# Kernel tuning notes

Measured on AMD Instinct MI355X. Metric: run time of the kernel, lower is better.

## Reference

```python
import jax, jax.numpy as jnp
import numpy as np

B = 262144
C = 128
NUM_CLASSES = 128   # fill_max for y
PAD = 2048
EPS = 1e-8
REJECT_THRESHOLD = 1


def setup_inputs() -> dict:
    key = jax.random.key(0)
    kx, ky = jax.random.split(key)
    x = jax.random.normal(kx, (B, C), dtype=jnp.float32)
    y = jax.random.randint(ky, (B,), 0, NUM_CLASSES)
    return {"x": x, "y": y}


def _decorrelate_loss(x, y):
    Bn, Cn = x.shape
    # per-class counts / sums (segment reduce replaces the python loop + boolean mask)
    counts = jax.ops.segment_sum(jnp.ones((Bn,), x.dtype), y, num_segments=NUM_CLASSES)  # [K]
    counts_i = counts.astype(jnp.int32)
    sums = jax.ops.segment_sum(x, y, num_segments=NUM_CLASSES)                            # [K, C]
    mean = sums / jnp.maximum(counts, 1.0)[:, None]
    centered = x - mean[y]                                                                # [B, C]
    # unbiased variance per class (torch .var default), guarded for count<=1
    var = jax.ops.segment_sum(centered * centered, y, num_segments=NUM_CLASSES) \
        / jnp.maximum(counts - 1.0, 1.0)[:, None]                                         # [K, C]
    xn = centered / jnp.sqrt(EPS + var)[y]                                                # [B, C]
    # sort rows by class so each class occupies a contiguous block, then slice fixed-size
    order = jnp.argsort(y)
    xs = jnp.concatenate([xn[order], jnp.zeros((PAD, Cn), x.dtype)], axis=0)              # [B+PAD, C]
    cum = jnp.cumsum(counts_i)
    starts = jnp.concatenate([jnp.zeros((1,), jnp.int32), cum[:-1]])                      # exclusive cumsum
    gathered = jax.vmap(lambda s: jax.lax.dynamic_slice(xs, (s, 0), (PAD, Cn)))(starts)   # [K, PAD, C]
    row_valid = (jnp.arange(PAD)[None, :] < counts_i[:, None]).astype(x.dtype)            # [K, PAD]
    g = gathered * row_valid[:, :, None]
    # per-class correlation matrices, all at once
    corr = jnp.einsum('kpc,kpd->kcd', g, g)                                               # [K, C, C]
    sq_sum = jnp.sum(corr * corr, axis=(1, 2))                                            # [K]
    diag_sq = jnp.sum(jnp.einsum('kcc->kc', corr) ** 2, axis=1)                           # [K]
    off_mean = (sq_sum - diag_sq) / (Cn * (Cn - 1))                                       # off_diagonal(.)^2 mean
    valid = counts_i > REJECT_THRESHOLD
    loss = jnp.sum(jnp.where(valid, off_mean, 0.0))
    n_count = jnp.sum(jnp.where(valid, counts, 0.0))
    return jnp.where(n_count > 0, loss / n_count, 0.0)


def reference(x, y):
    return _decorrelate_loss(x, y)
```

## Files before the change

### kernel.cpp

```cpp
#include <hip/hip_runtime.h>

#define B_ROWS   262144
#define C_DIM    128
#define K_CLS    128
#define PAD_R    2048
#define PAD2     4096
#define EPS_F    1e-8f
#define CHUNK    1024
#define G_CHUNKS 256

typedef float f32x4  __attribute__((ext_vector_type(4)));
typedef short bf16x8 __attribute__((ext_vector_type(8)));

__device__ __forceinline__ unsigned f2bf(float f) {
  unsigned u = __float_as_uint(f);
  return (u + 0x7fffu + ((u >> 16) & 1u)) >> 16;
}
__device__ __forceinline__ unsigned packbf(float a, float b) {
  return f2bf(a) | (f2bf(b) << 16);
}
__device__ __forceinline__ int swzkey(int c) { return (c ^ (c >> 2)) & 7; }

__global__ __launch_bounds__(256) void hist_kernel(const int* __restrict__ y,
                                                   int* __restrict__ hist) {
  __shared__ int h[K_CLS];
  int g = blockIdx.x, tid = threadIdx.x;
  if (tid < K_CLS) h[tid] = 0;
  __syncthreads();
  for (int j = tid; j < CHUNK; j += 256) atomicAdd(&h[y[g * CHUNK + j]], 1);
  __syncthreads();
  if (tid < K_CLS) hist[g * K_CLS + tid] = h[tid];
}

__global__ __launch_bounds__(256) void scan_kernel(int* __restrict__ hist,
                                                   int* __restrict__ counts) {
  __shared__ int s[G_CHUNKS];
  int k = blockIdx.x, g = threadIdx.x;
  int v = hist[g * K_CLS + k];
  s[g] = v;
  __syncthreads();
  for (int off = 1; off < G_CHUNKS; off <<= 1) {
    int t = (g >= off) ? s[g - off] : 0;
    __syncthreads();
    s[g] += t;
    __syncthreads();
  }
  hist[g * K_CLS + k] = s[g] - v;
  if (g == G_CHUNKS - 1) counts[k] = s[g];
}

__global__ __launch_bounds__(256) void rank_kernel(const int* __restrict__ y,
                                                   const int* __restrict__ hist,
                                                   int* __restrict__ ord) {
  __shared__ unsigned short cnt_sub[16][K_CLS];
  __shared__ int offs[K_CLS];
  const int g = blockIdx.x, tid = threadIdx.x;
  const int lane = tid & 63, w = tid >> 6;
  if (tid < K_CLS) offs[tid] = hist[g * K_CLS + tid];
  {
    unsigned int* cz = (unsigned int*)cnt_sub;
    for (int i = tid; i < 16 * K_CLS / 2; i += 256) cz[i] = 0;
  }
  __syncthreads();

  int yv[4], rig[4];
  #pragma unroll
  for (int i = 0; i < 4; ++i) {
    const int s = w * 4 + i;
    const int yy = y[g * CHUNK + s * 64 + lane];
    unsigned long long m = ~0ULL;
    #pragma unroll
    for (int b = 0; b < 7; ++b) {
      unsigned long long bb = __ballot((yy >> b) & 1);
      m &= ((yy >> b) & 1) ? bb : ~bb;
    }
    const unsigned long long lt = (1ULL << lane) - 1ULL;
    rig[i] = (int)__popcll(m & lt);
    yv[i] = yy;
    const int leader = __ffsll((long long)m) - 1;
    if (lane == leader) cnt_sub[s][yy] = (unsigned short)__popcll(m);
  }
  __syncthreads();

  if (tid < K_CLS) {
    int run = 0;
    #pragma unroll
    for (int s = 0; s < 16; ++s) {
      int t = cnt_sub[s][tid];
      cnt_sub[s][tid] = (unsigned short)run;
      run += t;
    }
  }
  __syncthreads();

  #pragma unroll
  for (int i = 0; i < 4; ++i) {
    const int s = w * 4 + i;
    const int k = yv[i];
    const int R = offs[k] + (int)cnt_sub[s][k] + rig[i];
    if (R < PAD2) ord[k * PAD2 + R] = g * CHUNK + s * 64 + lane;
  }
}

__global__ __launch_bounds__(512, 1) void gemm_kernel(const float* __restrict__ x,
                                                      const int* __restrict__ ord,
                                                      const int* __restrict__ counts,
                                                      float* __restrict__ spart,
                                                      float* __restrict__ sums_part,
                                                      float* __restrict__ sqs_part,
                                                      float* __restrict__ ovfs_part) {
  __shared__ unsigned int lds[2 * C_DIM * 32];
  __shared__ int ord_l[PAD_R / 2];
  const int blk = blockIdx.x;
  const int k = blk >> 1, half = blk & 1;
  const int cnt_full = counts[k];
  const int T = cnt_full < PAD_R ? cnt_full : PAD_R;
  const int r_base = half * (PAD_R / 2);
  const int rend = (T < r_base + PAD_R / 2) ? T : (r_base + PAD_R / 2);
  const int nr = rend - r_base;
  const int nt = (nr > 0) ? ((nr + 63) >> 6) : 0;

  const int tid = threadIdx.x;
  const int lane = tid & 63;
  const int w = tid >> 6;
  const int wr = w >> 1, wc = w & 1;
  const int l5 = lane >> 5;
  const int lc = lane & 31;

  f32x4 acc[2][4];
  #pragma unroll
  for (int i = 0; i < 2; ++i)
    #pragma unroll
    for (int j = 0; j < 4; ++j) acc[i][j] = (f32x4){0.f, 0.f, 0.f, 0.f};
  float sum4[4] = {0.f, 0.f, 0.f, 0.f}, sq4[4] = {0.f, 0.f, 0.f, 0.f};

  const int* ordk = ord + k * PAD2;

  for (int i = tid; i < PAD_R / 2; i += 512) ord_l[i] = ordk[r_base + i];
  __syncthreads();

  auto load_tile = [&](int t, f32x4* vv) {
    const int rr = t * 64 + w * 8 + l5 * 4;
    const int4 idx = *(const int4*)(&ord_l[rr]);
    const int rg = r_base + rr;
    const size_t co = (size_t)(lc << 2);
    const f32x4 z = (f32x4){0.f, 0.f, 0.f, 0.f};
    vv[0] = (rg + 0 < rend) ? *(const f32x4*)(x + (size_t)idx.x * C_DIM + co) : z;
    vv[1] = (rg + 1 < rend) ? *(const f32x4*)(x + (size_t)idx.y * C_DIM + co) : z;
    vv[2] = (rg + 2 < rend) ? *(const f32x4*)(x + (size_t)idx.z * C_DIM + co) : z;
    vv[3] = (rg + 3 < rend) ? *(const f32x4*)(x + (size_t)idx.w * C_DIM + co) : z;
  };

  auto write_tile = [&](unsigned int* buf, const f32x4* vv) {
    #pragma unroll
    for (int j = 0; j < 4; ++j)
      #pragma unroll
      for (int e = 0; e < 4; ++e) { float t = vv[j][e]; sum4[e] += t; sq4[e] += t * t; }
    #pragma unroll
    for (int jp = 0; jp < 2; ++jp) {
      const int us = l5 * 2 + jp;
      #pragma unroll
      for (int e = 0; e < 4; ++e) {
        const int c = (lc << 2) + e;
        buf[c * 32 + (((w ^ swzkey(c)) << 2) | us)] =
            packbf(vv[jp * 2][e], vv[jp * 2 + 1][e]);
      }
    }
  };

  auto compute_tile = [&](const unsigned int* buf) {
    const int q2 = lane >> 4;
    const int fr = lane & 15;
    #pragma unroll
    for (int s = 0; s < 2; ++s) {
      const int g = s * 4 + q2;
      bf16x8 afr[2], bfr[4];
      #pragma unroll
      for (int mi = 0; mi < 2; ++mi) {
        const int c = wr * 32 + mi * 16 + fr;
        afr[mi] = *(const bf16x8*)(&buf[c * 32 + ((g ^ swzkey(c)) << 2)]);
      }
      #pragma unroll
      for (int ni = 0; ni < 4; ++ni) {
        const int d = wc * 64 + ni * 16 + fr;
        bfr[ni] = *(const bf16x8*)(&buf[d * 32 + ((g ^ swzkey(d)) << 2)]);
      }
      #pragma unroll
      for (int mi = 0; mi < 2; ++mi)
        #pragma unroll
        for (int ni = 0; ni < 4; ++ni)
          acc[mi][ni] = __builtin_amdgcn_mfma_f32_16x16x32_bf16(afr[mi], bfr[ni], acc[mi][ni], 0, 0, 0);
    }
  };

  f32x4 va[4], vb[4];
  if (nt > 0) { load_tile(0, va); write_tile(lds, va); }
  if (nt > 1) load_tile(1, va);
  __syncthreads();
  int cur = 0;
  for (int t = 0; t < nt; t += 2) {
    if (t + 1 < nt) write_tile(lds + (unsigned)(cur ^ 1) * (C_DIM * 32), va);
    if (t + 2 < nt) load_tile(t + 2, vb);
    compute_tile(lds + (unsigned)cur * (C_DIM * 32));
    __syncthreads();
    cur ^= 1;
    if (t + 1 >= nt) break;
    if (t + 2 < nt) write_tile(lds + (unsigned)(cur ^ 1) * (C_DIM * 32), vb);
    if (t + 3 < nt) load_tile(t + 3, va);
    compute_tile(lds + (unsigned)cur * (C_DIM * 32));
    __syncthreads();
    cur ^= 1;
  }

  float osum[4] = {0.f, 0.f, 0.f, 0.f}, osq[4] = {0.f, 0.f, 0.f, 0.f};
  const int colo = lc << 2;
  for (int r = PAD_R + half + ((tid >> 5) << 1); r < cnt_full; r += 32) {
    int row = ordk[r];
    f32x4 vv = *(const f32x4*)(x + (size_t)row * C_DIM + colo);
    #pragma unroll
    for (int e = 0; e < 4; ++e) { float t = vv[e]; osum[e] += t; osq[e] += t * t; }
  }

  __syncthreads();
  float* red = (float*)lds;
  if (tid < 3 * C_DIM) red[tid] = 0.f;
  __syncthreads();
  #pragma unroll
  for (int e = 0; e < 4; ++e) {
    atomicAdd(&red[colo + e], sum4[e]);
    atomicAdd(&red[C_DIM + colo + e], sq4[e] + osq[e]);
    atomicAdd(&red[2 * C_DIM + colo + e], osum[e]);
  }
  __syncthreads();
  if (tid < C_DIM) {
    sums_part[(half * K_CLS + k) * C_DIM + tid] = red[tid];
    sqs_part [(half * K_CLS + k) * C_DIM + tid] = red[C_DIM + tid];
    ovfs_part[(half * K_CLS + k) * C_DIM + tid] = red[2 * C_DIM + tid];
  }
  float* sp = spart + (size_t)(half * K_CLS + k) * (C_DIM * C_DIM);
  #pragma unroll
  for (int mi = 0; mi < 2; ++mi)
    #pragma unroll
    for (int ni = 0; ni < 4; ++ni)
      #pragma unroll
      for (int r = 0; r < 4; ++r) {
        int c = wr * 32 + mi * 16 + ((lane >> 4) << 2) + r;
        int d = wc * 64 + ni * 16 + (lane & 15);
        sp[c * C_DIM + d] = acc[mi][ni][r];
      }
}

__global__ __launch_bounds__(512) void finalize_kernel(const float* __restrict__ spart,
                                                       const float* __restrict__ sums_part,
                                                       const float* __restrict__ sqs_part,
                                                       const float* __restrict__ ovfs_part,
                                                       const int* __restrict__ counts,
                                                       float* __restrict__ numden) {
  __shared__ float m_l[C_DIM], is_l[C_DIM], st_l[C_DIM];
  __shared__ float wred[8];
  int k = blockIdx.x, tid = threadIdx.x;
  int count = counts[k];
  float Tf = (float)(count < PAD_R ? count : PAD_R);
  if (tid < C_DIM) {
    float s_tr = sums_part[k * C_DIM + tid] + sums_part[(K_CLS + k) * C_DIM + tid];
    float osum = ovfs_part[k * C_DIM + tid] + ovfs_part[(K_CLS + k) * C_DIM + tid];
    float fsum = s_tr + osum;
    float fsq  = sqs_part[k * C_DIM + tid] + sqs_part[(K_CLS + k) * C_DIM + tid];
    float cf = (float)count;
    float m = fsum / fmaxf(cf, 1.f);
    float var = (fsq - cf * m * m) / fmaxf(cf - 1.f, 1.f);
    m_l[tid] = m;
    is_l[tid] = rsqrtf(var + EPS_F);
    st_l[tid] = s_tr;
  }
  __syncthreads();
  const float* S0 = spart + (size_t)k * (C_DIM * C_DIM);
  const float* S1 = spart + (size_t)(K_CLS + k) * (C_DIM * C_DIM);
  float local = 0.f;
  for (int e4 = tid * 4; e4 < C_DIM * C_DIM; e4 += 512 * 4) {
    int c = e4 >> 7, d0 = e4 & 127;
    f32x4 s0 = *(const f32x4*)(S0 + e4);
    f32x4 s1 = *(const f32x4*)(S1 + e4);
    #pragma unroll
    for (int e = 0; e < 4; ++e) {
      int d = d0 + e;
      float S = s0[e] + s1[e];
      float corr = is_l[c] * is_l[d] *
                   (S - m_l[c] * st_l[d] - m_l[d] * st_l[c] + Tf * m_l[c] * m_l[d]);
      if (c != d) local += corr * corr;
    }
  }
  for (int off = 32; off > 0; off >>= 1) local += __shfl_down(local, off);
  int lane = tid & 63, wid = tid >> 6;
  if (lane == 0) wred[wid] = local;
  __syncthreads();
  if (tid == 0 && count > 1) {
    float tot = 0.f;
    #pragma unroll
    for (int i = 0; i < 8; ++i) tot += wred[i];
    atomicAdd(&numden[0], tot * (1.f / (float)(C_DIM * (C_DIM - 1))));
    atomicAdd(&numden[1], (float)count);
  }
}

__global__ void div_kernel(const float* __restrict__ numden, float* __restrict__ out) {
  if (threadIdx.x == 0 && blockIdx.x == 0)
    out[0] = numden[1] > 0.f ? numden[0] / numden[1] : 0.f;
}

extern "C" void kernel_launch(void* const* d_in, const int* in_sizes, int n_in,
                              void* d_out, int out_size, void* d_ws, size_t ws_size,
                              hipStream_t stream) {
  (void)in_sizes; (void)n_in; (void)out_size; (void)ws_size;
  const float* x = (const float*)d_in[0];
  const int*   y = (const int*)d_in[1];
  float* out = (float*)d_out;
  char* ws = (char*)d_ws;

  float* numden    = (float*)(ws + 0);
  int*   hist      = (int*)(ws + 256);
  int*   counts    = (int*)(ws + 131328);
  int*   ord       = (int*)(ws + 132096);
  float* sums_part = (float*)(ws + 2229248);
  float* sqs_part  = (float*)(ws + 2360320);
  float* ovfs_part = (float*)(ws + 2491392);
  float* spart     = (float*)(ws + 2622464);

  (void)hipMemsetAsync(numden, 0, 256, stream);

  hist_kernel<<<G_CHUNKS, 256, 0, stream>>>(y, hist);
  scan_kernel<<<K_CLS, 256, 0, stream>>>(hist, counts);
  rank_kernel<<<G_CHUNKS, 256, 0, stream>>>(y, hist, ord);
  gemm_kernel<<<2 * K_CLS, 512, 0, stream>>>(x, ord, counts, spart, sums_part, sqs_part,
                                             ovfs_part);
  finalize_kernel<<<K_CLS, 512, 0, stream>>>(spart, sums_part, sqs_part, ovfs_part,
                                             counts, numden);
  div_kernel<<<1, 64, 0, stream>>>(numden, out);
}
```

Baseline: 64.96 us.

## Split per-class Gram accumulation across four blocks and fold memset into hist kernel

Each class's row range is now split into four quarters instead of two, so the gemm kernel launches 512 blocks instead of 256, and the launch bound is raised to allow more blocks per CU. The finalize kernel sums four partial Gram matrices and partial statistics instead of two. The numden memset is folded into the histogram kernel to save one launch. Row indices are clamped to stay in bounds. This should give better CU occupancy and latency hiding, in exchange for twice the partial-matrix write and read traffic in finalize and a tighter register budget.

Result: slower. 102.0 us (+57.0%).

```diff
diff --git a/kernel.cpp b/kernel.cpp
--- a/kernel.cpp
+++ b/kernel.cpp
@@ -5,6 +5,8 @@
 #define K_CLS    128
 #define PAD_R    2048
 #define PAD2     4096
+#define QSPLIT   4
+#define QROWS    (PAD_R / QSPLIT)
 #define EPS_F    1e-8f
 #define CHUNK    1024
 #define G_CHUNKS 256
@@ -22,9 +24,11 @@
 __device__ __forceinline__ int swzkey(int c) { return (c ^ (c >> 2)) & 7; }
 
 __global__ __launch_bounds__(256) void hist_kernel(const int* __restrict__ y,
-                                                   int* __restrict__ hist) {
+                                                   int* __restrict__ hist,
+                                                   float* __restrict__ numden) {
   __shared__ int h[K_CLS];
   int g = blockIdx.x, tid = threadIdx.x;
+  if (g == 0 && tid < 64) numden[tid] = 0.f;
   if (tid < K_CLS) h[tid] = 0;
   __syncthreads();
   for (int j = tid; j < CHUNK; j += 256) atomicAdd(&h[y[g * CHUNK + j]], 1);
@@ -102,7 +106,7 @@
   }
 }
 
-__global__ __launch_bounds__(512, 1) void gemm_kernel(const float* __restrict__ x,
+__global__ __launch_bounds__(512, 4) void gemm_kernel(const float* __restrict__ x,
                                                       const int* __restrict__ ord,
                                                       const int* __restrict__ counts,
                                                       float* __restrict__ spart,
@@ -110,13 +114,13 @@
                                                       float* __restrict__ sqs_part,
                                                       float* __restrict__ ovfs_part) {
   __shared__ unsigned int lds[2 * C_DIM * 32];
-  __shared__ int ord_l[PAD_R / 2];
+  __shared__ int ord_l[QROWS];
   const int blk = blockIdx.x;
-  const int k = blk >> 1, half = blk & 1;
+  const int k = blk >> 2, quarter = blk & 3;
   const int cnt_full = counts[k];
   const int T = cnt_full < PAD_R ? cnt_full : PAD_R;
-  const int r_base = half * (PAD_R / 2);
-  const int rend = (T < r_base + PAD_R / 2) ? T : (r_base + PAD_R / 2);
+  const int r_base = quarter * QROWS;
+  const int rend = (T < r_base + QROWS) ? T : (r_base + QROWS);
   const int nr = rend - r_base;
   const int nt = (nr > 0) ? ((nr + 63) >> 6) : 0;
 
@@ -136,7 +140,10 @@
 
   const int* ordk = ord + k * PAD2;
 
-  for (int i = tid; i < PAD_R / 2; i += 512) ord_l[i] = ordk[r_base + i];
+  for (int i = tid; i < QROWS; i += 512) {
+    int vi = ordk[r_base + i];
+    ord_l[i] = ((unsigned)vi < B_ROWS) ? vi : 0;
+  }
   __syncthreads();
 
   auto load_tile = [&](int t, f32x4* vv) {
@@ -214,7 +221,7 @@
 
   float osum[4] = {0.f, 0.f, 0.f, 0.f}, osq[4] = {0.f, 0.f, 0.f, 0.f};
   const int colo = lc << 2;
-  for (int r = PAD_R + half + ((tid >> 5) << 1); r < cnt_full; r += 32) {
+  for (int r = PAD_R + quarter + ((tid >> 5) << 2); r < cnt_full; r += 64) {
     int row = ordk[r];
     f32x4 vv = *(const f32x4*)(x + (size_t)row * C_DIM + colo);
     #pragma unroll
@@ -233,11 +240,11 @@
   }
   __syncthreads();
   if (tid < C_DIM) {
-    sums_part[(half * K_CLS + k) * C_DIM + tid] = red[tid];
-    sqs_part [(half * K_CLS + k) * C_DIM + tid] = red[C_DIM + tid];
-    ovfs_part[(half * K_CLS + k) * C_DIM + tid] = red[2 * C_DIM + tid];
-  }
-  float* sp = spart + (size_t)(half * K_CLS + k) * (C_DIM * C_DIM);
+    sums_part[(quarter * K_CLS + k) * C_DIM + tid] = red[tid];
+    sqs_part [(quarter * K_CLS + k) * C_DIM + tid] = red[C_DIM + tid];
+    ovfs_part[(quarter * K_CLS + k) * C_DIM + tid] = red[2 * C_DIM + tid];
+  }
+  float* sp = spart + (size_t)(quarter * K_CLS + k) * (C_DIM * C_DIM);
   #pragma unroll
   for (int mi = 0; mi < 2; ++mi)
     #pragma unroll
@@ -262,10 +269,14 @@
   int count = counts[k];
   float Tf = (float)(count < PAD_R ? count : PAD_R);
   if (tid < C_DIM) {
-    float s_tr = sums_part[k * C_DIM + tid] + sums_part[(K_CLS + k) * C_DIM + tid];
-    float osum = ovfs_part[k * C_DIM + tid] + ovfs_part[(K_CLS + k) * C_DIM + tid];
+    float s_tr = 0.f, osum = 0.f, fsq = 0.f;
+    #pragma unroll
+    for (int j = 0; j < QSPLIT; ++j) {
+      s_tr += sums_part[(j * K_CLS + k) * C_DIM + tid];
+      osum += ovfs_part[(j * K_CLS + k) * C_DIM + tid];
+      fsq  += sqs_part [(j * K_CLS + k) * C_DIM + tid];
+    }
     float fsum = s_tr + osum;
-    float fsq  = sqs_part[k * C_DIM + tid] + sqs_part[(K_CLS + k) * C_DIM + tid];
     float cf = (float)count;
     float m = fsum / fmaxf(cf, 1.f);
     float var = (fsq - cf * m * m) / fmaxf(cf - 1.f, 1.f);
@@ -274,19 +285,21 @@
     st_l[tid] = s_tr;
   }
   __syncthreads();
-  const float* S0 = spart + (size_t)k * (C_DIM * C_DIM);
-  const float* S1 = spart + (size_t)(K_CLS + k) * (C_DIM * C_DIM);
   float local = 0.f;
   for (int e4 = tid * 4; e4 < C_DIM * C_DIM; e4 += 512 * 4) {
     int c = e4 >> 7, d0 = e4 & 127;
-    f32x4 s0 = *(const f32x4*)(S0 + e4);
-    f32x4 s1 = *(const f32x4*)(S1 + e4);
+    f32x4 sa = (f32x4){0.f, 0.f, 0.f, 0.f};
+    #pragma unroll
+    for (int j = 0; j < QSPLIT; ++j) {
+      f32x4 sj = *(const f32x4*)(spart + (size_t)(j * K_CLS + k) * (C_DIM * C_DIM) + e4);
+      #pragma unroll
+      for (int e = 0; e < 4; ++e) sa[e] += sj[e];
+    }
     #pragma unroll
     for (int e = 0; e < 4; ++e) {
       int d = d0 + e;
-      float S = s0[e] + s1[e];
       float corr = is_l[c] * is_l[d] *
-                   (S - m_l[c] * st_l[d] - m_l[d] * st_l[c] + Tf * m_l[c] * m_l[d]);
+                   (sa[e] - m_l[c] * st_l[d] - m_l[d] * st_l[c] + Tf * m_l[c] * m_l[d]);
       if (c != d) local += corr * corr;
     }
   }
@@ -322,17 +335,15 @@
   int*   counts    = (int*)(ws + 131328);
   int*   ord       = (int*)(ws + 132096);
   float* sums_part = (float*)(ws + 2229248);
-  float* sqs_part  = (float*)(ws + 2360320);
-  float* ovfs_part = (float*)(ws + 2491392);
-  float* spart     = (float*)(ws + 2622464);
-
-  (void)hipMemsetAsync(numden, 0, 256, stream);
-
-  hist_kernel<<<G_CHUNKS, 256, 0, stream>>>(y, hist);
+  float* sqs_part  = (float*)(ws + 2491392);
+  float* ovfs_part = (float*)(ws + 2753536);
+  float* spart     = (float*)(ws + 3015680);
+
+  hist_kernel<<<G_CHUNKS, 256, 0, stream>>>(y, hist, numden);
   scan_kernel<<<K_CLS, 256, 0, stream>>>(hist, counts);
   rank_kernel<<<G_CHUNKS, 256, 0, stream>>>(y, hist, ord);
-  gemm_kernel<<<2 * K_CLS, 512, 0, stream>>>(x, ord, counts, spart, sums_part, sqs_part,
-                                             ovfs_part);
+  gemm_kernel<<<QSPLIT * K_CLS, 512, 0, stream>>>(x, ord, counts, spart, sums_part,
+                                                  sqs_part, ovfs_part);
   finalize_kernel<<<K_CLS, 512, 0, stream>>>(spart, sums_part, sqs_part, ovfs_part,
                                              counts, numden);
   div_kernel<<<1, 64, 0, stream>>>(numden, out);
```
